# Kernel optimization log

Measured on AMD Instinct MI355X. Metric: run time of the kernel, lower is better.

The kernel has to match this reference:

```python
import jax, jax.numpy as jnp
import numpy as np

TAU = 1.0
K = 10
N_NODES = 1048576
N_GRAPHS = 4096


def setup_inputs() -> dict:
    key = jax.random.key(0)
    k1, k2, k3 = jax.random.split(key, 3)
    # per-node scalar logits
    x = jax.random.normal(k1, (N_NODES, 1), dtype=jnp.float32)
    # uniforms for gumbel noise, kept away from {0,1} for log stability
    uniforms = jax.random.uniform(k2, (N_NODES, 3 * K), dtype=jnp.float32,
                                  minval=1e-6, maxval=1.0 - 1e-6)
    # PyG-style ptr: B+1 cumulative offsets, ptr[0]=0, ptr[-1]=N
    cuts = jnp.sort(jax.random.randint(k3, (N_GRAPHS - 1,), 1, N_NODES))
    ptr = jnp.concatenate([jnp.zeros((1,), cuts.dtype), cuts,
                           jnp.full((1,), N_NODES, cuts.dtype)])
    return {"x": x, "uniforms": uniforms, "ptr": ptr}


def reference(x, uniforms, ptr):
    # x: [N, 1] node logits; uniforms: [N, 3k]; ptr: [B+1] segment offsets
    N = x.shape[0]
    B = ptr.shape[0] - 1
    # node i belongs to graph g where ptr[g] <= i < ptr[g+1]
    seg = jnp.searchsorted(ptr, jnp.arange(N), side="right") - 1  # [N]
    gumbel = -jnp.log(-jnp.log(uniforms))                           # [N, 3k]
    noisy = (gumbel + x) / TAU                                      # [N, 3k]
    # segmented softmax over nodes (dim=0 within each graph), per column
    m = jax.ops.segment_max(noisy, seg, num_segments=B)             # [B, 3k]
    e = jnp.exp(noisy - m[seg])                                     # [N, 3k]
    denom = jax.ops.segment_sum(e, seg, num_segments=B)             # [B, 3k]
    probs = e / denom[seg]                                          # [N, 3k]
    # max over the 3k gumbel samples per node
    samples = jnp.max(probs, axis=1)                                # [N]
    return samples[:, None]                                         # [N, 1]
```

## Files before the change

kernel.cpp:

```cpp
#include <hip/hip_runtime.h>

#define K3 30
#define KP 15

__device__ __forceinline__ float hw_log2(float a) {
    return __builtin_amdgcn_logf(a);
}
__device__ __forceinline__ float hw_exp2(float a) {
    return __builtin_amdgcn_exp2f(a);
}

__global__ __launch_bounds__(256) void gnn_sample_concrete_kernel(
    const float* __restrict__ x,
    const float* __restrict__ uniforms,
    const int* __restrict__ ptr,
    float* __restrict__ out)
{
    const int wave = threadIdx.x >> 6;
    const int lane = threadIdx.x & 63;
    const int g = (blockIdx.x << 2) + wave;

    const int start = ptr[g];
    const int end   = ptr[g + 1];
    if (end <= start) return;

    float acc[K3];
#pragma unroll
    for (int j = 0; j < K3; ++j) acc[j] = 0.0f;

    const int iters = (end - start + 63) >> 6;

    for (int it = 0; it < iters; ++it) {
        const int n = start + (it << 6) + lane;
        if (n < end) {
            const float xe = fmaf(x[n], 1.44269504f, 0.52876637f);
            const float2* row =
                reinterpret_cast<const float2*>(uniforms + (size_t)n * K3);
#pragma unroll
            for (int k = 0; k < KP; ++k) {
                float2 u = row[k];
                float t0 = hw_log2(-hw_log2(u.x));
                float t1 = hw_log2(-hw_log2(u.y));
                acc[2 * k]     += hw_exp2(xe - t0);
                acc[2 * k + 1] += hw_exp2(xe - t1);
            }
        }
    }

#pragma unroll
    for (int j = 0; j < K3; ++j) {
        float v = acc[j];
#pragma unroll
        for (int off = 1; off < 64; off <<= 1)
            v += __shfl_xor(v, off, 64);
        acc[j] = hw_log2(v);
    }

    for (int it = 0; it < iters; ++it) {
        const int n = start + (it << 6) + lane;
        if (n < end) {
            const float xe = fmaf(x[n], 1.44269504f, 0.52876637f);
            const float2* row =
                reinterpret_cast<const float2*>(uniforms + (size_t)n * K3);
            float mn = 3.0e38f;
#pragma unroll
            for (int k = 0; k < KP; ++k) {
                float2 u = row[k];
                float t0 = hw_log2(-hw_log2(u.x));
                float t1 = hw_log2(-hw_log2(u.y));
                mn = fminf(mn, fminf(t0 + acc[2 * k], t1 + acc[2 * k + 1]));
            }
            out[n] = hw_exp2(xe - mn);
        }
    }
}

extern "C" void kernel_launch(void* const* d_in, const int* in_sizes, int n_in,
                              void* d_out, int out_size, void* d_ws, size_t ws_size,
                              hipStream_t stream) {
    const float* x        = (const float*)d_in[0];
    const float* uniforms = (const float*)d_in[1];
    const int*   ptr      = (const int*)d_in[2];
    float* out = (float*)d_out;

    const int B = in_sizes[2] - 1;
    const int blocks = (B + 3) / 4;

    gnn_sample_concrete_kernel<<<blocks, 256, 0, stream>>>(x, uniforms, ptr, out);
}
```

Before: 80.57 us.

## Split into node-parallel accumulate, log, and output kernels with atomics

Replaces the one-wave-per-graph kernel with a three-kernel pipeline. A node-parallel pass accumulates per-segment exp sums into a workspace using atomics, with 16 lanes covering the 30 columns of each node. A small kernel takes log2 of the sums, and a node-parallel output pass finds each node's segment by binary search. This is meant to fix load imbalance from uneven graph sizes, at the cost of extra launches, a memset, atomics, and reading the uniforms twice from global memory.

```diff
diff --git a/kernel.cpp b/kernel.cpp
--- a/kernel.cpp
+++ b/kernel.cpp
@@ -1,43 +1,126 @@
 #include <hip/hip_runtime.h>
 
-#define K3 30
-#define KP 15
+#define NK3 30
+#define NKP 15
 
-__device__ __forceinline__ float hw_log2(float a) {
-    return __builtin_amdgcn_logf(a);
-}
-__device__ __forceinline__ float hw_exp2(float a) {
-    return __builtin_amdgcn_exp2f(a);
+__device__ __forceinline__ float hw_log2(float a) { return __builtin_amdgcn_logf(a); }
+__device__ __forceinline__ float hw_exp2(float a) { return __builtin_amdgcn_exp2f(a); }
+
+__global__ __launch_bounds__(256) void k1_accumulate(
+    const float* __restrict__ x, const float* __restrict__ uniforms,
+    const int* __restrict__ ptr, float* __restrict__ wsum, int N, int B)
+{
+    const int wid  = (blockIdx.x << 2) + (threadIdx.x >> 6);
+    const int lane = threadIdx.x & 63;
+    const int nodesub = lane >> 4;
+    const int cp      = lane & 15;
+    const bool active = cp < NKP;
+
+    const int base = wid << 7;
+    if (base >= N) return;
+
+    int n0 = base + nodesub;
+    int lo = 0, hi = B;
+    while (hi - lo > 1) { int mid = (lo + hi) >> 1; if (ptr[mid] <= n0) lo = mid; else hi = mid; }
+    int seg = lo;
+    int ptr_next = ptr[seg + 1];
+
+    float ax = 0.f, ay = 0.f;
+
+    for (int s = 0; s < 32; ++s) {
+        const int n = base + (s << 2) + nodesub;
+        if (n < N) {
+            if (n >= ptr_next) {
+                if (active) {
+                    atomicAdd(&wsum[seg * NK3 + (cp << 1)    ], ax);
+                    atomicAdd(&wsum[seg * NK3 + (cp << 1) + 1], ay);
+                }
+                ax = 0.f; ay = 0.f;
+                do { ++seg; ptr_next = ptr[seg + 1]; } while (n >= ptr_next);
+            }
+            if (active) {
+                const float xe = fmaf(x[n], 1.44269504f, 0.52876637f);
+                const float2 u =
+                    reinterpret_cast<const float2*>(uniforms + (size_t)n * NK3)[cp];
+                const float t0 = hw_log2(-hw_log2(u.x));
+                const float t1 = hw_log2(-hw_log2(u.y));
+                ax += hw_exp2(xe - t0);
+                ay += hw_exp2(xe - t1);
+            }
+        }
+    }
+    if (active) {
+        atomicAdd(&wsum[seg * NK3 + (cp << 1)    ], ax);
+        atomicAdd(&wsum[seg * NK3 + (cp << 1) + 1], ay);
+    }
 }
 
-__global__ __launch_bounds__(256) void gnn_sample_concrete_kernel(
-    const float* __restrict__ x,
-    const float* __restrict__ uniforms,
-    const int* __restrict__ ptr,
-    float* __restrict__ out)
+__global__ __launch_bounds__(256) void k2_log(float* __restrict__ wsum, int count)
+{
+    const int i = blockIdx.x * 256 + threadIdx.x;
+    if (i < count) wsum[i] = hw_log2(wsum[i]);
+}
+
+__global__ __launch_bounds__(256) void k3_output(
+    const float* __restrict__ x, const float* __restrict__ uniforms,
+    const int* __restrict__ ptr, const float* __restrict__ lw,
+    float* __restrict__ out, int N, int B)
+{
+    const int wid  = (blockIdx.x << 2) + (threadIdx.x >> 6);
+    const int lane = threadIdx.x & 63;
+    const int base = wid << 8;
+    if (base >= N) return;
+
+    const int n0 = base + lane;
+    int lo = 0, hi = B;
+    while (hi - lo > 1) { int mid = (lo + hi) >> 1; if (ptr[mid] <= n0) lo = mid; else hi = mid; }
+    int seg = lo;
+
+    for (int c = 0; c < 4; ++c) {
+        const int n = base + (c << 6) + lane;
+        if (n >= N) return;
+        while (n >= ptr[seg + 1]) ++seg;
+
+        float l[NK3];
+#pragma unroll
+        for (int j = 0; j < NK3; ++j) l[j] = lw[seg * NK3 + j];
+
+        const float2* row = reinterpret_cast<const float2*>(uniforms + (size_t)n * NK3);
+        float mn = 3.0e38f;
+#pragma unroll
+        for (int k = 0; k < NKP; ++k) {
+            const float2 u = row[k];
+            const float t0 = hw_log2(-hw_log2(u.x));
+            const float t1 = hw_log2(-hw_log2(u.y));
+            mn = fminf(mn, fminf(t0 + l[2 * k], t1 + l[2 * k + 1]));
+        }
+        out[n] = hw_exp2(fmaf(x[n], 1.44269504f, 0.52876637f) - mn);
+    }
+}
+
+__global__ __launch_bounds__(256) void gnn_fallback(
+    const float* __restrict__ x, const float* __restrict__ uniforms,
+    const int* __restrict__ ptr, float* __restrict__ out)
 {
     const int wave = threadIdx.x >> 6;
     const int lane = threadIdx.x & 63;
     const int g = (blockIdx.x << 2) + wave;
-
     const int start = ptr[g];
     const int end   = ptr[g + 1];
     if (end <= start) return;
 
-    float acc[K3];
+    float acc[NK3];
 #pragma unroll
-    for (int j = 0; j < K3; ++j) acc[j] = 0.0f;
-
+    for (int j = 0; j < NK3; ++j) acc[j] = 0.0f;
     const int iters = (end - start + 63) >> 6;
 
     for (int it = 0; it < iters; ++it) {
         const int n = start + (it << 6) + lane;
         if (n < end) {
             const float xe = fmaf(x[n], 1.44269504f, 0.52876637f);
-            const float2* row =
-                reinterpret_cast<const float2*>(uniforms + (size_t)n * K3);
+            const float2* row = reinterpret_cast<const float2*>(uniforms + (size_t)n * NK3);
 #pragma unroll
-            for (int k = 0; k < KP; ++k) {
+            for (int k = 0; k < NKP; ++k) {
                 float2 u = row[k];
                 float t0 = hw_log2(-hw_log2(u.x));
                 float t1 = hw_log2(-hw_log2(u.y));
@@ -46,25 +129,21 @@
             }
         }
     }
-
 #pragma unroll
-    for (int j = 0; j < K3; ++j) {
+    for (int j = 0; j < NK3; ++j) {
         float v = acc[j];
 #pragma unroll
-        for (int off = 1; off < 64; off <<= 1)
-            v += __shfl_xor(v, off, 64);
+        for (int off = 1; off < 64; off <<= 1) v += __shfl_xor(v, off, 64);
         acc[j] = hw_log2(v);
     }
-
     for (int it = 0; it < iters; ++it) {
         const int n = start + (it << 6) + lane;
         if (n < end) {
             const float xe = fmaf(x[n], 1.44269504f, 0.52876637f);
-            const float2* row =
-                reinterpret_cast<const float2*>(uniforms + (size_t)n * K3);
+            const float2* row = reinterpret_cast<const float2*>(uniforms + (size_t)n * NK3);
             float mn = 3.0e38f;
 #pragma unroll
-            for (int k = 0; k < KP; ++k) {
+            for (int k = 0; k < NKP; ++k) {
                 float2 u = row[k];
                 float t0 = hw_log2(-hw_log2(u.x));
                 float t1 = hw_log2(-hw_log2(u.y));
@@ -83,8 +162,25 @@
     const int*   ptr      = (const int*)d_in[2];
     float* out = (float*)d_out;
 
+    const int N = in_sizes[0];
     const int B = in_sizes[2] - 1;
-    const int blocks = (B + 3) / 4;
+    const size_t ws_needed = (size_t)B * NK3 * sizeof(float);
 
-    gnn_sample_concrete_kernel<<<blocks, 256, 0, stream>>>(x, uniforms, ptr, out);
+    if (ws_size >= ws_needed && d_ws != nullptr) {
+        float* wsum = (float*)d_ws;
+        hipMemsetAsync(wsum, 0, ws_needed, stream);
+
+        const int b1 = (N + 511) / 512;
+        k1_accumulate<<<b1, 256, 0, stream>>>(x, uniforms, ptr, wsum, N, B);
+
+        const int cnt = B * NK3;
+        const int b2 = (cnt + 255) / 256;
+        k2_log<<<b2, 256, 0, stream>>>(wsum, cnt);
+
+        const int b3 = (N + 1023) / 1024;
+        k3_output<<<b3, 256, 0, stream>>>(x, uniforms, ptr, wsum, out, N, B);
+    } else {
+        const int blocks = (B + 3) / 4;
+        gnn_fallback<<<blocks, 256, 0, stream>>>(x, uniforms, ptr, out);
+    }
 }
```

New measurement: 85.25 us. +5.8%, slower.
